# Kernel tuning notes

Hardware: AMD Instinct MI355X
Metric: run time of the kernel (lower is better)

## Reference

```python
import jax, jax.numpy as jnp
import numpy as np

B, H, W, C = 4, 180, 320, 64
ATTN_SCALE = 0.125  # C ** -0.5
EPS = 1e-6  # flax LayerNorm default epsilon


def _layer_norm(x, scale, bias):
    mu = jnp.mean(x, axis=-1, keepdims=True)
    var = jnp.mean(jnp.square(x - mu), axis=-1, keepdims=True)
    return (x - mu) * jax.lax.rsqrt(var + EPS) * scale + bias


def setup_inputs() -> dict:
    key = jax.random.key(0)
    ks = jax.random.split(key, 8)
    w_init = 1.0 / np.sqrt(C)  # lecun_normal-ish scale for CxC dense kernels
    return {
        "x_l": jax.random.normal(ks[0], (B, H, W, C), jnp.float32),
        "x_r": jax.random.normal(ks[1], (B, H, W, C), jnp.float32),
        "ln_l_scale": jnp.ones((C,), jnp.float32),
        "ln_l_bias": jnp.zeros((C,), jnp.float32),
        "ln_r_scale": jnp.ones((C,), jnp.float32),
        "ln_r_bias": jnp.zeros((C,), jnp.float32),
        "w_ql": jax.random.normal(ks[2], (C, C), jnp.float32) * w_init,
        "b_ql": jnp.zeros((C,), jnp.float32),
        "w_qr": jax.random.normal(ks[3], (C, C), jnp.float32) * w_init,
        "b_qr": jnp.zeros((C,), jnp.float32),
        "w_vl": jax.random.normal(ks[4], (C, C), jnp.float32) * w_init,
        "b_vl": jnp.zeros((C,), jnp.float32),
        "w_vr": jax.random.normal(ks[5], (C, C), jnp.float32) * w_init,
        "b_vr": jnp.zeros((C,), jnp.float32),
        "beta": jax.random.normal(ks[6], (1, 1, 1, C), jnp.float32) * 0.1,
        "gamma": jax.random.normal(ks[7], (1, 1, 1, C), jnp.float32) * 0.1,
    }


def reference(x_l, x_r, ln_l_scale, ln_l_bias, ln_r_scale, ln_r_bias,
              w_ql, b_ql, w_qr, b_qr, w_vl, b_vl, w_vr, b_vr, beta, gamma):
    # Projections (attention runs along the width axis, per (b, h) scanline)
    q_l = _layer_norm(x_l, ln_l_scale, ln_l_bias) @ w_ql + b_ql   # [B,H,W,C]
    q_r = _layer_norm(x_r, ln_r_scale, ln_r_bias) @ w_qr + b_qr   # [B,H,W,C]
    v_l = x_l @ w_vl + b_vl                                       # [B,H,W,C]
    v_r = x_r @ w_vr + b_vr                                       # [B,H,W,C]

    # Shared score matrix: [B, H, W_l, W_r]
    attn = jnp.einsum('bhlc,bhrc->bhlr', q_l, q_r) * ATTN_SCALE

    # Row softmax (over W_r) attends right->left
    f_r2l = jnp.einsum('bhlr,bhrc->bhlc', jax.nn.softmax(attn, axis=-1), v_r) * beta
    # Column softmax (over W_l) attends left->right
    f_l2r = jnp.einsum('bhlr,bhlc->bhrc', jax.nn.softmax(attn, axis=-2), v_l) * gamma

    return (x_l + f_r2l, x_r + f_l2r)
```

## Files before the change

### kernel.cpp

```cpp
#include <hip/hip_runtime.h>
#include <hip/hip_bf16.h>

#define NB 4
#define NH 180
#define NW 320
#define NC 64
#define NSCAN (NB*NH)
#define NROWS (NB*NH*NW)
#define NELEM ((size_t)NROWS*NC)

using short8  = __attribute__((ext_vector_type(8))) short;
using floatx4 = __attribute__((ext_vector_type(4))) float;
using uint2v  = __attribute__((ext_vector_type(2))) unsigned int;

__device__ __forceinline__ unsigned short fbf(float f) {
    __hip_bfloat16 h = __float2bfloat16(f);
    unsigned short s; __builtin_memcpy(&s, &h, 2); return s;
}
__device__ __forceinline__ unsigned int packbf(float lo, float hi) {
    return (unsigned int)fbf(lo) | ((unsigned int)fbf(hi) << 16);
}

__device__ __forceinline__ void swap32(unsigned& a, unsigned& b, int lane) {
#if __has_builtin(__builtin_amdgcn_permlane32_swap)
    uint2v r = __builtin_amdgcn_permlane32_swap(a, b, false, false);
    a = r.x; b = r.y;
#else
    unsigned as = __shfl_xor(a, 32), bs = __shfl_xor(b, 32);
    unsigned na = (lane < 32) ? a : bs;
    unsigned nb = (lane < 32) ? as : b;
    a = na; b = nb;
#endif
}
__device__ __forceinline__ void swap16(unsigned& a, unsigned& b, int lane) {
#if __has_builtin(__builtin_amdgcn_permlane16_swap)
    uint2v r = __builtin_amdgcn_permlane16_swap(a, b, false, false);
    a = r.x; b = r.y;
#else
    unsigned as = __shfl_xor(a, 16), bs = __shfl_xor(b, 16);
    unsigned na = (lane & 16) ? bs : a;
    unsigned nb = (lane & 16) ? b : as;
    a = na; b = nb;
#endif
}

#define SCALE_LOG2E 0.18033688011112042f

__global__ __launch_bounds__(256) void proj_kernel(
    const float* __restrict__ xl, const float* __restrict__ xr,
    const float* __restrict__ lsl, const float* __restrict__ lbl,
    const float* __restrict__ lsr, const float* __restrict__ lbr,
    const float* __restrict__ wql, const float* __restrict__ bql,
    const float* __restrict__ wqr, const float* __restrict__ bqr,
    const float* __restrict__ wvl, const float* __restrict__ bvl,
    const float* __restrict__ wvr, const float* __restrict__ bvr,
    __hip_bfloat16* __restrict__ ql, __hip_bfloat16* __restrict__ qr,
    __hip_bfloat16* __restrict__ vlT, __hip_bfloat16* __restrict__ vrT)
{
    const int flat = blockIdx.x + 900 * blockIdx.y;
    const int g    = (flat & 7) * 450 + (flat >> 3);
    const int kind = g & 1;
    const int pairid = g >> 1;
    const int side = pairid & 1;
    const int tile = pairid >> 1;
    const int p    = side + 2 * kind;
    const int t    = threadIdx.x;
    const int row0 = tile * 256;

    const float* src  = (p == 0 || p == 2) ? xl : xr;
    const float* Wm   = (p == 0) ? wql : (p == 1) ? wqr : (p == 2) ? wvl : wvr;
    const float* bias = (p == 0) ? bql : (p == 1) ? bqr : (p == 2) ? bvl : bvr;
    __hip_bfloat16* dst = (p == 0) ? ql : (p == 1) ? qr : (p == 2) ? vlT : vrT;
    const bool doLN = (p < 2);
    const float* lns = (p == 0) ? lsl : lsr;
    const float* lnb = (p == 0) ? lbl : lbr;
    const float oscale = (p == 0) ? SCALE_LOG2E : 1.0f;

    __shared__ __align__(16) __hip_bfloat16 sA[256 * 72];
    __shared__ __align__(16) __hip_bfloat16 sWt[64 * 72];
    __shared__ float sLs[64], sLb[64], sBias[64];

    if (t < 64) {
        sLs[t]   = doLN ? lns[t] : 1.0f;
        sLb[t]   = doLN ? lnb[t] : 0.0f;
        sBias[t] = bias[t];
    }
    {
        const int k  = t >> 2;
        const int c0 = (t & 3) * 16;
        const float4* wrow = (const float4*)(Wm + k * NC + c0);
        float wv[16];
#pragma unroll
        for (int j = 0; j < 4; ++j) {
            float4 w4 = wrow[j];
            wv[4*j] = w4.x; wv[4*j+1] = w4.y; wv[4*j+2] = w4.z; wv[4*j+3] = w4.w;
        }
#pragma unroll
        for (int j = 0; j < 16; ++j)
            sWt[(c0 + j) * 72 + k] = __float2bfloat16(wv[j]);
    }
    __syncthreads();

    {
        const float4* x4 = (const float4*)(src + (size_t)(row0 + t) * NC);
        float f[64];
#pragma unroll
        for (int j = 0; j < 16; ++j) {
            float4 v = x4[j];
            f[4*j] = v.x; f[4*j+1] = v.y; f[4*j+2] = v.z; f[4*j+3] = v.w;
        }
        if (doLN) {
            float s = 0.f, s2 = 0.f;
#pragma unroll
            for (int c = 0; c < 64; ++c) { s += f[c]; s2 = fmaf(f[c], f[c], s2); }
            const float mu   = s * (1.0f / 64.0f);
            const float var  = s2 * (1.0f / 64.0f) - mu * mu;
            const float rstd = rsqrtf(var + 1e-6f);
#pragma unroll
            for (int c = 0; c < 64; ++c) f[c] = (f[c] - mu) * rstd * sLs[c] + sLb[c];
        }
        unsigned int* arow = (unsigned int*)&sA[t * 72];
#pragma unroll
        for (int j = 0; j < 32; ++j) arow[j] = packbf(f[2*j], f[2*j+1]);
    }
    __syncthreads();

    const int lane = t & 63;
    const int wv_  = t >> 6;
    const int quad = lane >> 4;
    const int mn   = lane & 15;

    short8 bfr[4][2];
#pragma unroll
    for (int nt = 0; nt < 4; ++nt)
#pragma unroll
        for (int ks = 0; ks < 2; ++ks)
            bfr[nt][ks] = *(const short8*)&sWt[(nt * 16 + mn) * 72 + ks * 32 + quad * 8];

#pragma unroll
    for (int mt = 0; mt < 4; ++mt) {
        const int rl = wv_ * 64 + mt * 16 + mn;
        short8 a0 = *(const short8*)&sA[rl * 72 +      quad * 8];
        short8 a1 = *(const short8*)&sA[rl * 72 + 32 + quad * 8];
#pragma unroll
        for (int nt = 0; nt < 4; ++nt) {
            floatx4 c = {0.f, 0.f, 0.f, 0.f};
            c = __builtin_amdgcn_mfma_f32_16x16x32_bf16(a0, bfr[nt][0], c, 0, 0, 0);
            c = __builtin_amdgcn_mfma_f32_16x16x32_bf16(a1, bfr[nt][1], c, 0, 0, 0);
            const int col = nt * 16 + mn;
            const float bb = sBias[col];
            if (p < 2) {
#pragma unroll
                for (int i = 0; i < 4; ++i) {
                    const int rowl = wv_ * 64 + mt * 16 + quad * 4 + i;
                    dst[(size_t)(row0 + rowl) * NC + col] =
                        __float2bfloat16((c[i] + bb) * oscale);
                }
            } else {
#pragma unroll
                for (int i = 0; i < 4; ++i) {
                    const unsigned grow = (unsigned)(row0 + wv_ * 64 + mt * 16 + quad * 4 + i);
                    const unsigned sc   = grow / 320u;
                    const unsigned wr   = grow - sc * 320u;
                    dst[(size_t)sc * (NC * NW) + (unsigned)col * NW + wr] =
                        __float2bfloat16(c[i] + bb);
                }
            }
        }
    }
}

__global__ __launch_bounds__(256, 6) void attn_kernel(
    const __hip_bfloat16* __restrict__ ql, const __hip_bfloat16* __restrict__ qr,
    const __hip_bfloat16* __restrict__ vlT, const __hip_bfloat16* __restrict__ vrT,
    const float* __restrict__ xl, const float* __restrict__ xr,
    const float* __restrict__ beta, const float* __restrict__ gamma,
    float* __restrict__ out)
{
    const int flat = blockIdx.x + 5 * (blockIdx.y + 720 * blockIdx.z);
    const int g    = (flat & 7) * 900 + (flat >> 3);
    const int mt   = g % 5;
    const int s2   = g / 5;
    const int p    = s2 & 1;
    const int scan = s2 >> 1;

    const int t    = threadIdx.x;
    const int lane = t & 63;
    const int w    = t >> 6;
    const int quad = lane >> 4;
    const int mn   = lane & 15;
    const int m0   = mt * 64;

    const __hip_bfloat16* Q  = (p ? qr  : ql ) + (size_t)scan * (NW * NC);
    const __hip_bfloat16* K  = (p ? ql  : qr ) + (size_t)scan * (NW * NC);
    const __hip_bfloat16* VT = (p ? vlT : vrT) + (size_t)scan * (NC * NW);
    const float* xS = p ? xr : xl;
    const float* gv = p ? gamma : beta;

    __shared__ __align__(16) char sU[18432];
    __shared__ float sRS[64];
    __hip_bfloat16* sK  = (__hip_bfloat16*)sU;
    __hip_bfloat16* sVt = (__hip_bfloat16*)(sU + 9216);
    float* sO = (float*)sU;

    const int sr  = t >> 2;
    const int sc0 = (t & 3) * 16;

    uint4 rk0, rk1, rv0, rv1;
    {
        const uint4* gk = (const uint4*)(K + (size_t)sr * NC + sc0);
        rk0 = gk[0]; rk1 = gk[1];
        const uint4* gt = (const uint4*)(VT + (size_t)sr * NW + sc0);
        rv0 = gt[0]; rv1 = gt[1];
    }

    const __hip_bfloat16* qrow = Q + (size_t)(m0 + w * 16 + mn) * NC;
    const short8 qa0 = *(const short8*)(qrow + quad * 8);
    const short8 qa1 = *(const short8*)(qrow + 32 + quad * 8);

    floatx4 acc[4];
#pragma unroll
    for (int nt = 0; nt < 4; ++nt) acc[nt] = (floatx4){0.f, 0.f, 0.f, 0.f};
    float rs = 0.f;

    for (int rb = 0; rb < NW; rb += 64) {
        __syncthreads();
        {
            uint4* dk = (uint4*)&sK [sr * 72 + sc0]; dk[0] = rk0; dk[1] = rk1;
            uint4* dv = (uint4*)&sVt[sr * 72 + sc0]; dv[0] = rv0; dv[1] = rv1;
        }
        __syncthreads();

        if (rb + 64 < NW) {
            const uint4* gk = (const uint4*)(K + (size_t)(rb + 64 + sr) * NC + sc0);
            rk0 = gk[0]; rk1 = gk[1];
            const uint4* gt = (const uint4*)(VT + (size_t)sr * NW + (rb + 64) + sc0);
            rv0 = gt[0]; rv1 = gt[1];
        }

        __builtin_amdgcn_s_setprio(1);
        unsigned w0[4], w1[4];
#pragma unroll
        for (int rt = 0; rt < 4; ++rt) {
            short8 ka0 = *(const short8*)&sK[(rt * 16 + mn) * 72 +      quad * 8];
            short8 ka1 = *(const short8*)&sK[(rt * 16 + mn) * 72 + 32 + quad * 8];
            floatx4 s = {0.f, 0.f, 0.f, 0.f};
            s = __builtin_amdgcn_mfma_f32_16x16x32_bf16(ka0, qa0, s, 0, 0, 0);
            s = __builtin_amdgcn_mfma_f32_16x16x32_bf16(ka1, qa1, s, 0, 0, 0);
            const float e0 = exp2f(s[0]), e1 = exp2f(s[1]);
            const float e2 = exp2f(s[2]), e3 = exp2f(s[3]);
            rs += (e0 + e1) + (e2 + e3);
            w0[rt] = packbf(e0, e1);
            w1[rt] = packbf(e2, e3);
        }

#pragma unroll
        for (int ks = 0; ks < 2; ++ks) {
            unsigned a0 = w0[2 * ks], b0 = w0[2 * ks + 1];
            swap32(a0, b0, lane); swap16(a0, b0, lane);
            unsigned a1 = w1[2 * ks], b1 = w1[2 * ks + 1];
            swap32(a1, b1, lane); swap16(a1, b1, lane);
            uint4 pu; pu.x = a0; pu.y = a1; pu.z = b0; pu.w = b1;
            short8 pa; __builtin_memcpy(&pa, &pu, 16);
#pragma unroll
            for (int nt = 0; nt < 4; ++nt) {
                short8 vb = *(const short8*)&sVt[(nt * 16 + mn) * 72 + ks * 32 + quad * 8];
                acc[nt] = __builtin_amdgcn_mfma_f32_16x16x32_bf16(pa, vb, acc[nt], 0, 0, 0);
            }
        }
        __builtin_amdgcn_s_setprio(0);
    }

    rs += __shfl_xor(rs, 16);
    rs += __shfl_xor(rs, 32);

    __syncthreads();

    if (lane < 16) sRS[w * 16 + lane] = 1.0f / rs;
#pragma unroll
    for (int nt = 0; nt < 4; ++nt)
#pragma unroll
        for (int i = 0; i < 4; ++i)
            sO[(w * 16 + quad * 4 + i) * 68 + nt * 16 + mn] = acc[nt][i];

    {
        const int m = t >> 2, c0 = (t & 3) * 16;
        const float inv = sRS[m];
        const int grow = scan * NW + m0 + m;
        const float4* xg = (const float4*)(xS + (size_t)grow * NC + c0);
        const float4* gg = (const float4*)(gv + c0);
        const float4* so = (const float4*)&sO[m * 68 + c0];
        float4* og = (float4*)(out + (p ? NELEM : (size_t)0) + (size_t)grow * NC + c0);
#pragma unroll
        for (int j = 0; j < 4; ++j) {
            float4 xv = xg[j];
            float4 gvv = gg[j];
            float4 ov = so[j];
            float4 o;
            o.x = xv.x + ov.x * inv * gvv.x;
            o.y = xv.y + ov.y * inv * gvv.y;
            o.z = xv.z + ov.z * inv * gvv.z;
            o.w = xv.w + ov.w * inv * gvv.w;
            og[j] = o;
        }
    }
}

extern "C" void kernel_launch(void* const* d_in, const int* in_sizes, int n_in,
                              void* d_out, int out_size, void* d_ws, size_t ws_size,
                              hipStream_t stream)
{
    const float* xl  = (const float*)d_in[0];
    const float* xr  = (const float*)d_in[1];
    const float* lsl = (const float*)d_in[2];
    const float* lbl = (const float*)d_in[3];
    const float* lsr = (const float*)d_in[4];
    const float* lbr = (const float*)d_in[5];
    const float* wql = (const float*)d_in[6];
    const float* bql = (const float*)d_in[7];
    const float* wqr = (const float*)d_in[8];
    const float* bqr = (const float*)d_in[9];
    const float* wvl = (const float*)d_in[10];
    const float* bvl = (const float*)d_in[11];
    const float* wvr = (const float*)d_in[12];
    const float* bvr = (const float*)d_in[13];
    const float* beta  = (const float*)d_in[14];
    const float* gamma = (const float*)d_in[15];

    __hip_bfloat16* ws   = (__hip_bfloat16*)d_ws;
    __hip_bfloat16* ql_  = ws;
    __hip_bfloat16* qr_  = ws + NELEM;
    __hip_bfloat16* vlT_ = ws + 2 * NELEM;
    __hip_bfloat16* vrT_ = ws + 3 * NELEM;

    proj_kernel<<<dim3(900, 4, 1), 256, 0, stream>>>(
        xl, xr, lsl, lbl, lsr, lbr, wql, bql, wqr, bqr, wvl, bvl, wvr, bvr,
        ql_, qr_, vlT_, vrT_);

    attn_kernel<<<dim3(5, NSCAN, 2), 256, 0, stream>>>(
        ql_, qr_, vlT_, vrT_, xl, xr, beta, gamma, (float*)d_out);
}
```

Measured before the change: 364.0 us.

## Merge both attention directions into one 512-thread block per scanline tile

Each block now handles both the left-to-right and right-to-left directions for the same scanline and 64-row tile. Eight waves are split four per direction, and each direction has its own K/V LDS buffers. The merge halves the grid and doubles LDS per block; the wider block may reduce occupancy or add barrier stalls. Softmax exponentials also switch to the hardware exp2 builtin to avoid the libm wrapper.

```diff
diff --git a/kernel.cpp b/kernel.cpp
--- a/kernel.cpp
+++ b/kernel.cpp
@@ -20,6 +20,12 @@
 __device__ __forceinline__ unsigned int packbf(float lo, float hi) {
     return (unsigned int)fbf(lo) | ((unsigned int)fbf(hi) << 16);
 }
+
+#if __has_builtin(__builtin_amdgcn_exp2f)
+#define EXP2(x) __builtin_amdgcn_exp2f(x)
+#else
+#define EXP2(x) exp2f(x)
+#endif
 
 __device__ __forceinline__ void swap32(unsigned& a, unsigned& b, int lane) {
 #if __has_builtin(__builtin_amdgcn_permlane32_swap)
@@ -170,51 +176,51 @@
     }
 }
 
-__global__ __launch_bounds__(256, 6) void attn_kernel(
+__global__ __launch_bounds__(512, 8) void attn_kernel(
     const __hip_bfloat16* __restrict__ ql, const __hip_bfloat16* __restrict__ qr,
     const __hip_bfloat16* __restrict__ vlT, const __hip_bfloat16* __restrict__ vrT,
     const float* __restrict__ xl, const float* __restrict__ xr,
     const float* __restrict__ beta, const float* __restrict__ gamma,
     float* __restrict__ out)
 {
-    const int flat = blockIdx.x + 5 * (blockIdx.y + 720 * blockIdx.z);
-    const int g    = (flat & 7) * 900 + (flat >> 3);
+    const int flat = blockIdx.x + 5 * blockIdx.y;
+    const int g    = (flat & 7) * 450 + (flat >> 3);
     const int mt   = g % 5;
-    const int s2   = g / 5;
-    const int p    = s2 & 1;
-    const int scan = s2 >> 1;
+    const int scan = g / 5;
 
     const int t    = threadIdx.x;
     const int lane = t & 63;
     const int w    = t >> 6;
+    const int dir  = w >> 2;
+    const int wl   = w & 3;
     const int quad = lane >> 4;
     const int mn   = lane & 15;
     const int m0   = mt * 64;
 
-    const __hip_bfloat16* Q  = (p ? qr  : ql ) + (size_t)scan * (NW * NC);
-    const __hip_bfloat16* K  = (p ? ql  : qr ) + (size_t)scan * (NW * NC);
-    const __hip_bfloat16* VT = (p ? vlT : vrT) + (size_t)scan * (NC * NW);
-    const float* xS = p ? xr : xl;
-    const float* gv = p ? gamma : beta;
-
-    __shared__ __align__(16) char sU[18432];
-    __shared__ float sRS[64];
-    __hip_bfloat16* sK  = (__hip_bfloat16*)sU;
-    __hip_bfloat16* sVt = (__hip_bfloat16*)(sU + 9216);
-    float* sO = (float*)sU;
-
-    const int sr  = t >> 2;
-    const int sc0 = (t & 3) * 16;
-
-    uint4 rk0, rk1, rv0, rv1;
-    {
-        const uint4* gk = (const uint4*)(K + (size_t)sr * NC + sc0);
-        rk0 = gk[0]; rk1 = gk[1];
-        const uint4* gt = (const uint4*)(VT + (size_t)sr * NW + sc0);
-        rv0 = gt[0]; rv1 = gt[1];
-    }
-
-    const __hip_bfloat16* qrow = Q + (size_t)(m0 + w * 16 + mn) * NC;
+    const __hip_bfloat16* K0g = qr  + (size_t)scan * (NW * NC);
+    const __hip_bfloat16* K1g = ql  + (size_t)scan * (NW * NC);
+    const __hip_bfloat16* V0g = vrT + (size_t)scan * (NC * NW);
+    const __hip_bfloat16* V1g = vlT + (size_t)scan * (NC * NW);
+    const __hip_bfloat16* Qg  = (dir ? qr : ql) + (size_t)scan * (NW * NC);
+
+    __shared__ __align__(16) char sU[36864];
+    __shared__ float sRS[128];
+    __hip_bfloat16* sK0 = (__hip_bfloat16*)(sU);
+    __hip_bfloat16* sK1 = (__hip_bfloat16*)(sU +  9216);
+    __hip_bfloat16* sV0 = (__hip_bfloat16*)(sU + 18432);
+    __hip_bfloat16* sV1 = (__hip_bfloat16*)(sU + 27648);
+    __hip_bfloat16* sKw = dir ? sK1 : sK0;
+    __hip_bfloat16* sVw = dir ? sV1 : sV0;
+
+    const int sr  = t >> 3;
+    const int sc0 = (t & 7) * 8;
+
+    uint4 rK0 = *(const uint4*)(K0g + (size_t)sr * NC + sc0);
+    uint4 rK1 = *(const uint4*)(K1g + (size_t)sr * NC + sc0);
+    uint4 rV0 = *(const uint4*)(V0g + (size_t)sr * NW + sc0);
+    uint4 rV1 = *(const uint4*)(V1g + (size_t)sr * NW + sc0);
+
+    const __hip_bfloat16* qrow = Qg + (size_t)(m0 + wl * 16 + mn) * NC;
     const short8 qa0 = *(const short8*)(qrow + quad * 8);
     const short8 qa1 = *(const short8*)(qrow + 32 + quad * 8);
 
@@ -226,29 +232,31 @@
     for (int rb = 0; rb < NW; rb += 64) {
         __syncthreads();
         {
-            uint4* dk = (uint4*)&sK [sr * 72 + sc0]; dk[0] = rk0; dk[1] = rk1;
-            uint4* dv = (uint4*)&sVt[sr * 72 + sc0]; dv[0] = rv0; dv[1] = rv1;
+            *(uint4*)&sK0[sr * 72 + sc0] = rK0;
+            *(uint4*)&sK1[sr * 72 + sc0] = rK1;
+            *(uint4*)&sV0[sr * 72 + sc0] = rV0;
+            *(uint4*)&sV1[sr * 72 + sc0] = rV1;
         }
         __syncthreads();
 
         if (rb + 64 < NW) {
-            const uint4* gk = (const uint4*)(K + (size_t)(rb + 64 + sr) * NC + sc0);
-            rk0 = gk[0]; rk1 = gk[1];
-            const uint4* gt = (const uint4*)(VT + (size_t)sr * NW + (rb + 64) + sc0);
-            rv0 = gt[0]; rv1 = gt[1];
+            rK0 = *(const uint4*)(K0g + (size_t)(rb + 64 + sr) * NC + sc0);
+            rK1 = *(const uint4*)(K1g + (size_t)(rb + 64 + sr) * NC + sc0);
+            rV0 = *(const uint4*)(V0g + (size_t)sr * NW + (rb + 64) + sc0);
+            rV1 = *(const uint4*)(V1g + (size_t)sr * NW + (rb + 64) + sc0);
         }
 
         __builtin_amdgcn_s_setprio(1);
         unsigned w0[4], w1[4];
 #pragma unroll
         for (int rt = 0; rt < 4; ++rt) {
-            short8 ka0 = *(const short8*)&sK[(rt * 16 + mn) * 72 +      quad * 8];
-            short8 ka1 = *(const short8*)&sK[(rt * 16 + mn) * 72 + 32 + quad * 8];
+            short8 ka0 = *(const short8*)&sKw[(rt * 16 + mn) * 72 +      quad * 8];
+            short8 ka1 = *(const short8*)&sKw[(rt * 16 + mn) * 72 + 32 + quad * 8];
             floatx4 s = {0.f, 0.f, 0.f, 0.f};
             s = __builtin_amdgcn_mfma_f32_16x16x32_bf16(ka0, qa0, s, 0, 0, 0);
             s = __builtin_amdgcn_mfma_f32_16x16x32_bf16(ka1, qa1, s, 0, 0, 0);
-            const float e0 = exp2f(s[0]), e1 = exp2f(s[1]);
-            const float e2 = exp2f(s[2]), e3 = exp2f(s[3]);
+            const float e0 = EXP2(s[0]), e1 = EXP2(s[1]);
+            const float e2 = EXP2(s[2]), e3 = EXP2(s[3]);
             rs += (e0 + e1) + (e2 + e3);
             w0[rt] = packbf(e0, e1);
             w1[rt] = packbf(e2, e3);
@@ -264,7 +272,7 @@
             short8 pa; __builtin_memcpy(&pa, &pu, 16);
 #pragma unroll
             for (int nt = 0; nt < 4; ++nt) {
-                short8 vb = *(const short8*)&sVt[(nt * 16 + mn) * 72 + ks * 32 + quad * 8];
+                short8 vb = *(const short8*)&sVw[(nt * 16 + mn) * 72 + ks * 32 + quad * 8];
                 acc[nt] = __builtin_amdgcn_mfma_f32_16x16x32_bf16(pa, vb, acc[nt], 0, 0, 0);
             }
         }
@@ -276,21 +284,28 @@
 
     __syncthreads();
 
-    if (lane < 16) sRS[w * 16 + lane] = 1.0f / rs;
+    if (lane < 16) sRS[dir * 64 + wl * 16 + lane] = 1.0f / rs;
+
+    float* sOw = (float*)(sU + dir * 17408);
 #pragma unroll
     for (int nt = 0; nt < 4; ++nt)
 #pragma unroll
         for (int i = 0; i < 4; ++i)
-            sO[(w * 16 + quad * 4 + i) * 68 + nt * 16 + mn] = acc[nt][i];
+            sOw[(wl * 16 + quad * 4 + i) * 68 + nt * 16 + mn] = acc[nt][i];
 
     {
-        const int m = t >> 2, c0 = (t & 3) * 16;
-        const float inv = sRS[m];
+        const int d  = t >> 8;
+        const int m  = (t & 255) >> 2;
+        const int c0 = (t & 3) * 16;
+        const float inv = sRS[d * 64 + m];
+        const float* xS = d ? xr : xl;
+        const float* gvp = d ? gamma : beta;
+        const float* sOd = (const float*)(sU + d * 17408);
         const int grow = scan * NW + m0 + m;
         const float4* xg = (const float4*)(xS + (size_t)grow * NC + c0);
-        const float4* gg = (const float4*)(gv + c0);
-        const float4* so = (const float4*)&sO[m * 68 + c0];
-        float4* og = (float4*)(out + (p ? NELEM : (size_t)0) + (size_t)grow * NC + c0);
+        const float4* gg = (const float4*)(gvp + c0);
+        const float4* so = (const float4*)(sOd + m * 68 + c0);
+        float4* og = (float4*)(out + (size_t)d * NELEM + (size_t)grow * NC + c0);
 #pragma unroll
         for (int j = 0; j < 4; ++j) {
             float4 xv = xg[j];
@@ -337,6 +352,6 @@
         xl, xr, lsl, lbl, lsr, lbr, wql, bql, wqr, bqr, wvl, bvl, wvr, bvr,
         ql_, qr_, vlT_, vrT_);
 
-    attn_kernel<<<dim3(5, NSCAN, 2), 256, 0, stream>>>(
+    attn_kernel<<<dim3(5, NSCAN, 1), 512, 0, stream>>>(
         ql_, qr_, vlT_, vrT_, xl, xr, beta, gamma, (float*)d_out);
 }
```

Result: slower. 556.8 us (+53.0%).

## Double-buffer K/V tiles in LDS and vectorize transposed V stores

Applied to the files above, without the earlier changes.

The attention loop now uses two LDS buffers for the K and transposed-V tiles. Each iteration writes the next tile into the spare buffer while computing on the current one, and prefetches two tiles ahead into registers. This cuts the per-iteration barriers from two to one. The V-transpose store in the projection kernel now writes four consecutive bf16 values as one ushort4 instead of four scalar stores. The cost is double the shared memory per block, which may lower occupancy under the 6-blocks-per-CU launch bound. The vector store also assumes the four rows never cross a scanline boundary, which holds because 320 is a multiple of 4.

```diff
diff --git a/kernel.cpp b/kernel.cpp
--- a/kernel.cpp
+++ b/kernel.cpp
@@ -157,14 +157,13 @@
                         __float2bfloat16((c[i] + bb) * oscale);
                 }
             } else {
-#pragma unroll
-                for (int i = 0; i < 4; ++i) {
-                    const unsigned grow = (unsigned)(row0 + wv_ * 64 + mt * 16 + quad * 4 + i);
-                    const unsigned sc   = grow / 320u;
-                    const unsigned wr   = grow - sc * 320u;
-                    dst[(size_t)sc * (NC * NW) + (unsigned)col * NW + wr] =
-                        __float2bfloat16(c[i] + bb);
-                }
+                const unsigned grow0 = (unsigned)(row0 + wv_ * 64 + mt * 16 + quad * 4);
+                const unsigned sc    = grow0 / 320u;
+                const unsigned wr0   = grow0 - sc * 320u;
+                ushort4 st;
+                st.x = fbf(c[0] + bb); st.y = fbf(c[1] + bb);
+                st.z = fbf(c[2] + bb); st.w = fbf(c[3] + bb);
+                *(ushort4*)&dst[(size_t)sc * (NC * NW) + (unsigned)col * NW + wr0] = st;
             }
         }
     }
@@ -197,10 +196,8 @@
     const float* xS = p ? xr : xl;
     const float* gv = p ? gamma : beta;
 
-    __shared__ __align__(16) char sU[18432];
+    __shared__ __align__(16) char sU[2][18432];
     __shared__ float sRS[64];
-    __hip_bfloat16* sK  = (__hip_bfloat16*)sU;
-    __hip_bfloat16* sVt = (__hip_bfloat16*)(sU + 9216);
     float* sO = (float*)sU;
 
     const int sr  = t >> 2;
@@ -213,28 +210,47 @@
         const uint4* gt = (const uint4*)(VT + (size_t)sr * NW + sc0);
         rv0 = gt[0]; rv1 = gt[1];
     }
+    {
+        __hip_bfloat16* sK0 = (__hip_bfloat16*)(sU[0]);
+        __hip_bfloat16* sV0 = (__hip_bfloat16*)(sU[0] + 9216);
+        uint4* dk = (uint4*)&sK0[sr * 72 + sc0]; dk[0] = rk0; dk[1] = rk1;
+        uint4* dv = (uint4*)&sV0[sr * 72 + sc0]; dv[0] = rv0; dv[1] = rv1;
+    }
+    {
+        const uint4* gk = (const uint4*)(K + (size_t)(64 + sr) * NC + sc0);
+        rk0 = gk[0]; rk1 = gk[1];
+        const uint4* gt = (const uint4*)(VT + (size_t)sr * NW + 64 + sc0);
+        rv0 = gt[0]; rv1 = gt[1];
+    }
 
     const __hip_bfloat16* qrow = Q + (size_t)(m0 + w * 16 + mn) * NC;
     const short8 qa0 = *(const short8*)(qrow + quad * 8);
     const short8 qa1 = *(const short8*)(qrow + 32 + quad * 8);
 
+    __syncthreads();
+
     floatx4 acc[4];
 #pragma unroll
     for (int nt = 0; nt < 4; ++nt) acc[nt] = (floatx4){0.f, 0.f, 0.f, 0.f};
     float rs = 0.f;
 
-    for (int rb = 0; rb < NW; rb += 64) {
-        __syncthreads();
-        {
-            uint4* dk = (uint4*)&sK [sr * 72 + sc0]; dk[0] = rk0; dk[1] = rk1;
-            uint4* dv = (uint4*)&sVt[sr * 72 + sc0]; dv[0] = rv0; dv[1] = rv1;
-        }
-        __syncthreads();
-
-        if (rb + 64 < NW) {
-            const uint4* gk = (const uint4*)(K + (size_t)(rb + 64 + sr) * NC + sc0);
+#pragma unroll
+    for (int i = 0; i < 5; ++i) {
+        const int c = i & 1;
+        const __hip_bfloat16* sK = (const __hip_bfloat16*)(sU[c]);
+        const __hip_bfloat16* sV = (const __hip_bfloat16*)(sU[c] + 9216);
+
+        if (i + 1 < 5) {
+            __hip_bfloat16* nK = (__hip_bfloat16*)(sU[c ^ 1]);
+            __hip_bfloat16* nV = (__hip_bfloat16*)(sU[c ^ 1] + 9216);
+            uint4* dk = (uint4*)&nK[sr * 72 + sc0]; dk[0] = rk0; dk[1] = rk1;
+            uint4* dv = (uint4*)&nV[sr * 72 + sc0]; dv[0] = rv0; dv[1] = rv1;
+        }
+        if (i + 2 < 5) {
+            const int rb2 = (i + 2) * 64;
+            const uint4* gk = (const uint4*)(K + (size_t)(rb2 + sr) * NC + sc0);
             rk0 = gk[0]; rk1 = gk[1];
-            const uint4* gt = (const uint4*)(VT + (size_t)sr * NW + (rb + 64) + sc0);
+            const uint4* gt = (const uint4*)(VT + (size_t)sr * NW + rb2 + sc0);
             rv0 = gt[0]; rv1 = gt[1];
         }
 
@@ -264,19 +280,20 @@
             short8 pa; __builtin_memcpy(&pa, &pu, 16);
 #pragma unroll
             for (int nt = 0; nt < 4; ++nt) {
-                short8 vb = *(const short8*)&sVt[(nt * 16 + mn) * 72 + ks * 32 + quad * 8];
+                short8 vb = *(const short8*)&sV[(nt * 16 + mn) * 72 + ks * 32 + quad * 8];
                 acc[nt] = __builtin_amdgcn_mfma_f32_16x16x32_bf16(pa, vb, acc[nt], 0, 0, 0);
             }
         }
         __builtin_amdgcn_s_setprio(0);
+
+        __syncthreads();
     }
 
     rs += __shfl_xor(rs, 16);
     rs += __shfl_xor(rs, 32);
 
-    __syncthreads();
-
     if (lane < 16) sRS[w * 16 + lane] = 1.0f / rs;
+
 #pragma unroll
     for (int nt = 0; nt < 4; ++nt)
 #pragma unroll
```

New measurement: 359.3 us. About the same (-1.3%).
